# Performance work log

Measured on AMD Instinct MI355X. Metric: run time of the kernel, lower is better.

The kernel has to match this reference:

```python
import jax, jax.numpy as jnp
import numpy as np


def setup_inputs() -> dict:
    key = jax.random.key(0)
    ks = jax.random.split(key, 7)
    OUT, IN, K = 4096, 4096, 2048
    U_STORED, VT_STORED = 512, 1024  # int(0.5*(K//2+1)), int(0.5*(IN//2+1))
    return {
        "x": jax.random.normal(ks[0], (1024, IN), dtype=jnp.float32),
        "U_real": jax.random.normal(ks[1], (OUT, U_STORED), dtype=jnp.float32) * 0.01,
        "U_imag": jax.random.normal(ks[2], (OUT, U_STORED), dtype=jnp.float32) * 0.01,
        "S": jax.random.normal(ks[3], (K,), dtype=jnp.float32) * 0.02,
        "Vt_real": jax.random.normal(ks[4], (K, VT_STORED), dtype=jnp.float32) * 0.01,
        "Vt_imag": jax.random.normal(ks[5], (K, VT_STORED), dtype=jnp.float32) * 0.01,
        "bias": jnp.zeros((OUT,), dtype=jnp.float32),
    }


def _decompress(coeffs_real, coeffs_imag, n):
    # Zero-pad truncated rfft coefficients back to n//2+1, then inverse rfft.
    c = jax.lax.complex(coeffs_real, coeffs_imag)
    num_unique = n // 2 + 1
    pad = num_unique - c.shape[-1]
    if pad > 0:
        c = jnp.pad(c, ((0, 0), (0, pad)))
    elif pad < 0:
        c = c[..., :num_unique]
    return jnp.fft.irfft(c, n=n, axis=-1)


def reference(x, U_real, U_imag, S, Vt_real, Vt_imag, bias):
    k_rank = S.shape[0]
    in_features = x.shape[-1]
    U = _decompress(U_real, U_imag, k_rank)            # (out, k)
    Vh = _decompress(Vt_real, Vt_imag, in_features)    # (k, in)
    W = (U * S[None, :]) @ Vh                          # (out, in) reconstructed weight
    return x @ W.T + bias                              # F.linear(x, W, bias)
```

## Files before the change

kernel.cpp:

```cpp
#include <hip/hip_runtime.h>
#include <math.h>
#include <stdint.h>

#define PI2 6.28318530717958647692f

typedef __bf16 bf16x8 __attribute__((ext_vector_type(8)));
typedef float f32x4 __attribute__((ext_vector_type(4)));

typedef __attribute__((address_space(1))) const void gvoid_t;
typedef __attribute__((address_space(3))) void lvoid_t;

__device__ __forceinline__ void g2l16(const void* g, void* l) {
    __builtin_amdgcn_global_load_lds(
        reinterpret_cast<gvoid_t*>(reinterpret_cast<uintptr_t>(g)),
        reinterpret_cast<lvoid_t*>(reinterpret_cast<uintptr_t>(l)),
        16, 0, 0);
}

__device__ __forceinline__ short f2bf(float f) {
    unsigned u = __float_as_uint(f);
    u += 0x7FFFu + ((u >> 16) & 1u);
    return (short)(u >> 16);
}

__device__ __forceinline__ unsigned pack2bf(float a, float b) {
    return (unsigned)(unsigned short)f2bf(a) |
           ((unsigned)(unsigned short)f2bf(b) << 16);
}

__device__ __forceinline__ float bflo(unsigned v) { return __uint_as_float(v << 16); }
__device__ __forceinline__ float bfhi(unsigned v) { return __uint_as_float(v & 0xFFFF0000u); }

__device__ __forceinline__ int xcd_swizzle(int blk, int G) {
    return (blk & 7) * (G >> 3) + (blk >> 3);
}

__global__ __launch_bounds__(256) void aux_all8(
    const float* __restrict__ x,
    const float* __restrict__ Ur, const float* __restrict__ Ui,
    const float* __restrict__ S,
    const float* __restrict__ Vr, const float* __restrict__ Vi,
    short* __restrict__ xe, short* __restrict__ xo,
    short* __restrict__ B1f, short* __restrict__ VcatT,
    short* __restrict__ B2, short* __restrict__ Ucat)
{
    __shared__ float tlds[64][68];
    const int b   = (int)blockIdx.x;
    const int tid = threadIdx.x;

    if (b < 1024) {
        unsigned i = (b * 256u + tid) * 8u;
        int r = i >> 11, j0 = i & 2047;
        const float* xr = x + (size_t)r * 4096 + j0;
        float4 a0 = ((const float4*)xr)[0], a1 = ((const float4*)xr)[1];
        float4 b0 = ((const float4*)(xr + 2048))[0],
               b1 = ((const float4*)(xr + 2048))[1];
        uint4 oe = {pack2bf(a0.x + b0.x, a0.y + b0.y),
                    pack2bf(a0.z + b0.z, a0.w + b0.w),
                    pack2bf(a1.x + b1.x, a1.y + b1.y),
                    pack2bf(a1.z + b1.z, a1.w + b1.w)};
        *(uint4*)(xe + i) = oe;
        uint4 oo = {pack2bf(a0.x - b0.x, a0.y - b0.y),
                    pack2bf(a0.z - b0.z, a0.w - b0.w),
                    pack2bf(a1.x - b1.x, a1.y - b1.y),
                    pack2bf(a1.z - b1.z, a1.w - b1.w)};
        *(uint4*)(xo + i) = oo;
    } else if (b < 3072) {
        unsigned i = ((b - 1024) * 256u + tid) * 8u;
        int r = i >> 11, j0 = i & 2047;
        const float inv_n = 1.0f / 4096.0f;
        float v[8];
        if (r < 512) {
            if (r == 0) {
                #pragma unroll
                for (int u = 0; u < 8; ++u) v[u] = inv_n;
            } else {
                #pragma unroll
                for (int u = 0; u < 8; ++u) {
                    int t = (r * (j0 + u)) & 2047;
                    v[u] = 2.0f * inv_n * cosf((float)t * (PI2 / 2048.0f));
                }
            }
        } else if (r < 1024) {
            int m = r - 512;
            #pragma unroll
            for (int u = 0; u < 8; ++u) {
                int t = (m * (j0 + u)) & 2047;
                v[u] = -2.0f * inv_n * sinf((float)t * (PI2 / 2048.0f));
            }
        } else if (r < 1536) {
            int c = 2 * (r - 1024) + 1;
            #pragma unroll
            for (int u = 0; u < 8; ++u) {
                int t = (c * (j0 + u)) & 4095;
                v[u] = 2.0f * inv_n * cosf((float)t * (PI2 / 4096.0f));
            }
        } else {
            int m = 2 * (r - 1536) + 1;
            #pragma unroll
            for (int u = 0; u < 8; ++u) {
                int t = (m * (j0 + u)) & 4095;
                v[u] = -2.0f * inv_n * sinf((float)t * (PI2 / 4096.0f));
            }
        }
        uint4 o = {pack2bf(v[0], v[1]), pack2bf(v[2], v[3]),
                   pack2bf(v[4], v[5]), pack2bf(v[6], v[7])};
        *(uint4*)(B1f + i) = o;
    } else if (b < 4096) {
        const int bb  = b - 3072;
        const int m   = bb >> 9;
        const int tt  = bb & 511;
        const int tkk = tt >> 4;
        const int tc  = tt & 15;
        const float* src = (m ? Vi : Vr) + (size_t)(tkk * 64) * 1024 + tc * 64;

        #pragma unroll
        for (int pass = 0; pass < 4; ++pass) {
            int r  = pass * 16 + (tid >> 4);
            int cq = (tid & 15) * 4;
            float4 v = *(const float4*)(src + (size_t)r * 1024 + cq);
            *(float4*)&tlds[r][cq] = v;
        }
        __syncthreads();

        const int cl = tid & 63;
        const int ch = (tid >> 6) * 16;
        const int c  = tc * 64 + cl;
        const int f  = ((c & 1) << 10) + (m << 9) + (c >> 1);
        float vv[16];
        #pragma unroll
        for (int j = 0; j < 16; ++j) vv[j] = tlds[ch + j][cl];
        uint4 o0 = {pack2bf(vv[0],  vv[1]),  pack2bf(vv[2],  vv[3]),
                    pack2bf(vv[4],  vv[5]),  pack2bf(vv[6],  vv[7])};
        uint4 o1 = {pack2bf(vv[8],  vv[9]),  pack2bf(vv[10], vv[11]),
                    pack2bf(vv[12], vv[13]), pack2bf(vv[14], vv[15])};
        uint4* dst = (uint4*)(VcatT + (size_t)f * 2048 + tkk * 64 + ch);
        dst[0] = o0;
        dst[1] = o1;
    } else if (b < 5120) {
        unsigned i = ((b - 4096) * 256u + tid) * 8u;
        int p = i >> 11, k0 = i & 2047;
        float4 s0 = *(const float4*)(S + k0);
        float4 s1 = *(const float4*)(S + k0 + 4);
        float sv[8] = {s0.x, s0.y, s0.z, s0.w, s1.x, s1.y, s1.z, s1.w};
        const float inv_n = 1.0f / 2048.0f;
        float v[8];
        if (p == 0) {
            #pragma unroll
            for (int u = 0; u < 8; ++u) v[u] = inv_n * sv[u];
        } else if (p < 512) {
            #pragma unroll
            for (int u = 0; u < 8; ++u) {
                int t = (p * (k0 + u)) & 2047;
                v[u] = 2.0f * inv_n * cosf((float)t * (PI2 / 2048.0f)) * sv[u];
            }
        } else {
            int q = p - 512;
            #pragma unroll
            for (int u = 0; u < 8; ++u) {
                int t = (q * (k0 + u)) & 2047;
                v[u] = -2.0f * inv_n * sinf((float)t * (PI2 / 2048.0f)) * sv[u];
            }
        }
        uint4 o = {pack2bf(v[0], v[1]), pack2bf(v[2], v[3]),
                   pack2bf(v[4], v[5]), pack2bf(v[6], v[7])};
        *(uint4*)(B2 + i) = o;
    } else {
        unsigned i = ((b - 5120) * 256u + tid) * 8u;
        int o_ = i >> 10, c = i & 1023;
        const float* src = (c < 512) ? (Ur + (size_t)o_ * 512 + c)
                                     : (Ui + (size_t)o_ * 512 + (c - 512));
        float4 a = ((const float4*)src)[0], bq = ((const float4*)src)[1];
        uint4 o = {pack2bf(a.x, a.y), pack2bf(a.z, a.w),
                   pack2bf(bq.x, bq.y), pack2bf(bq.z, bq.w)};
        *(uint4*)(Ucat + i) = o;
    }
}

__device__ __forceinline__ void tile_core(
    const short* __restrict__ A, int lda,
    const short* __restrict__ B, int ldb, int K,
    short* As, short* Bs, int bm, int bn, f32x4 (&acc)[4][4])
{
    const int tid  = threadIdx.x;
    const int wave = tid >> 6;
    const int lane = tid & 63;
    const int wm   = (wave >> 1) << 6;
    const int wn   = (wave & 1) << 6;
    const int l16  = lane & 15;
    const int quad = lane >> 4;
    const int rk   = l16 & 7;

    int aoff[4], boff[4], loff[4];
    #pragma unroll
    for (int p = 0; p < 4; ++p) {
        int L   = p * 256 + wave * 64 + lane;
        int row = L >> 3;
        int swz = (L & 7) ^ (row & 7);
        aoff[p] = (bm + row) * lda + swz * 8;
        boff[p] = (bn + row) * ldb + swz * 8;
        loff[p] = L * 8;
    }

    #pragma unroll
    for (int p = 0; p < 4; ++p) g2l16(A + aoff[p], As + loff[p]);
    #pragma unroll
    for (int p = 0; p < 4; ++p) g2l16(B + boff[p], Bs + loff[p]);
    __syncthreads();

    int cur = 0;
    for (int k0 = 0; k0 < K; k0 += 64) {
        const int nxt = cur ^ 1;
        if (k0 + 64 < K) {
            #pragma unroll
            for (int p = 0; p < 4; ++p)
                g2l16(A + aoff[p] + k0 + 64, As + nxt * 8192 + loff[p]);
            #pragma unroll
            for (int p = 0; p < 4; ++p)
                g2l16(B + boff[p] + k0 + 64, Bs + nxt * 8192 + loff[p]);
        }

        const short* Asc = As + cur * 8192;
        const short* Bsc = Bs + cur * 8192;
        #pragma unroll
        for (int h = 0; h < 2; ++h) {
            const int cs8 = ((((h << 2) | quad) ^ rk) << 3);
            bf16x8 b[4];
            #pragma unroll
            for (int nt = 0; nt < 4; ++nt)
                b[nt] = *(const bf16x8*)(Bsc + (wn + nt * 16 + l16) * 64 + cs8);
            #pragma unroll
            for (int mt = 0; mt < 4; ++mt) {
                bf16x8 a = *(const bf16x8*)(Asc + (wm + mt * 16 + l16) * 64 + cs8);
                #pragma unroll
                for (int nt = 0; nt < 4; ++nt)
                    acc[mt][nt] = __builtin_amdgcn_mfma_f32_16x16x32_bf16(
                        a, b[nt], acc[mt][nt], 0, 0, 0);
            }
        }
        __syncthreads();
        cur = nxt;
    }
}

__device__ __forceinline__ void store_tile_bf16(
    f32x4 (&acc)[4][4], short* __restrict__ C, int ldc, int bm, int bn)
{
    const int tid  = threadIdx.x;
    const int wave = tid >> 6;
    const int lane = tid & 63;
    const int wm   = (wave >> 1) << 6;
    const int wn   = (wave & 1) << 6;
    const int l16  = lane & 15;
    const int quad = lane >> 4;
    #pragma unroll
    for (int nt = 0; nt < 4; ++nt) {
        int col = bn + wn + nt * 16 + l16;
        #pragma unroll
        for (int mt = 0; mt < 4; ++mt) {
            int rowb = bm + wm + mt * 16 + quad * 4;
            #pragma unroll
            for (int r = 0; r < 4; ++r)
                C[(size_t)(rowb + r) * ldc + col] = f2bf(acc[mt][nt][r]);
        }
    }
}

__device__ __forceinline__ void store_frag(
    f32x4 (&acc)[4][4], short* __restrict__ planeTile)
{
    uint4* p = (uint4*)planeTile;
    const int tid = threadIdx.x;
    #pragma unroll
    for (int c = 0; c < 8; ++c) {
        int nt = c >> 1, mt0 = (c & 1) * 2;
        uint4 o = {pack2bf(acc[mt0][nt][0],     acc[mt0][nt][1]),
                   pack2bf(acc[mt0][nt][2],     acc[mt0][nt][3]),
                   pack2bf(acc[mt0 + 1][nt][0], acc[mt0 + 1][nt][1]),
                   pack2bf(acc[mt0 + 1][nt][2], acc[mt0 + 1][nt][3])};
        p[c * 256 + tid] = o;
    }
}

template <bool OUT_F32>
__device__ __forceinline__ void reduce_unit(
    const short* __restrict__ P, size_t planeU4, int SK,
    int tile, int c, int tilesX, void* __restrict__ Out, int ldc,
    const float* __restrict__ bias)
{
    const int bm = (tile / tilesX) << 7;
    const int bn = (tile % tilesX) << 7;
    const int tid  = threadIdx.x;
    const int wave = tid >> 6;
    const int lane = tid & 63;
    const int wm   = (wave >> 1) << 6;
    const int wn   = (wave & 1) << 6;
    const int l16  = lane & 15;
    const int quad = lane >> 4;
    const int nt   = c >> 1, mt0 = (c & 1) * 2;

    const uint4* P4 = (const uint4*)P;
    const size_t base = (size_t)tile * 2048 + (size_t)c * 256 + tid;
    float f[8] = {0, 0, 0, 0, 0, 0, 0, 0};
    for (int z = 0; z < SK; ++z) {
        uint4 v = P4[(size_t)z * planeU4 + base];
        f[0] += bflo(v.x); f[1] += bfhi(v.x);
        f[2] += bflo(v.y); f[3] += bfhi(v.y);
        f[4] += bflo(v.z); f[5] += bfhi(v.z);
        f[6] += bflo(v.w); f[7] += bfhi(v.w);
    }
    const int col = bn + wn + nt * 16 + l16;
    float bv = 0.f;
    if (OUT_F32) bv = bias[col];
    #pragma unroll
    for (int j = 0; j < 8; ++j) {
        int mt  = mt0 + (j >> 2);
        int row = bm + wm + mt * 16 + quad * 4 + (j & 3);
        if (OUT_F32)
            ((float*)Out)[(size_t)row * ldc + col] = f[j] + bv;
        else
            ((short*)Out)[(size_t)row * ldc + col] = f2bf(f[j]);
    }
}

__global__ __launch_bounds__(256, 2) void gemm_s1w2(
    const short* __restrict__ xe, const short* __restrict__ xo,
    const short* __restrict__ B1f,
    const short* __restrict__ B2, const short* __restrict__ VcatT,
    short* __restrict__ P, short* __restrict__ PW)
{
    __shared__ __align__(16) short As[2 * 128 * 64];
    __shared__ __align__(16) short Bs[2 * 128 * 64];

    f32x4 acc[4][4];
    #pragma unroll
    for (int i = 0; i < 4; ++i)
        #pragma unroll
        for (int j = 0; j < 4; ++j)
            acc[i][j] = (f32x4){0.f, 0.f, 0.f, 0.f};

    const int raw = (int)blockIdx.x;
    if (raw < 512) {
        const int u    = xcd_swizzle(raw, 512);
        const int z    = u >> 7;
        const int tile = u & 127;
        const int tx   = tile & 15, ty = tile >> 4;
        const bool odd = (tx & 8) != 0;
        const short* A = (odd ? xo : xe) + (size_t)z * 512;
        const short* B = B1f + (odd ? (size_t)1024 * 2048 : 0) + (size_t)z * 512;
        const int bm   = ty << 7;
        const int bn   = (tx & 7) << 7;

        tile_core(A, 2048, B, 2048, 512, As, Bs, bm, bn, acc);
        store_frag(acc, P + (size_t)z * 2097152 + (size_t)tile * 16384);
    } else {
        const int u    = xcd_swizzle(raw - 512, 512);
        const int z    = u >> 7;
        const int tile = u & 127;
        const int bm   = (tile >> 4) << 7;
        const int bn   = (tile & 15) << 7;

        tile_core(B2 + (size_t)z * 512, 2048, VcatT + (size_t)z * 512, 2048,
                  512, As, Bs, bm, bn, acc);
        store_frag(acc, PW + (size_t)z * 2097152 + (size_t)tile * 16384);
    }
}

__global__ __launch_bounds__(256) void reduce_s1w2(
    const short* __restrict__ P, const short* __restrict__ PW,
    short* __restrict__ Xp, short* __restrict__ W2)
{
    const int b   = (int)blockIdx.x;
    const int sub = b & 1023;
    if (b < 1024)
        reduce_unit<false>(P,  (size_t)2097152 >> 3, 4, sub >> 3, sub & 7,
                           16, Xp, 2048, nullptr);
    else
        reduce_unit<false>(PW, (size_t)2097152 >> 3, 4, sub >> 3, sub & 7,
                           16, W2, 2048, nullptr);
}

__global__ __launch_bounds__(256, 2) void gemm_sk_frag(
    const short* __restrict__ A, int lda,
    const short* __restrict__ B, int ldb,
    short* __restrict__ P, size_t planeShorts, int Kpart,
    int tileShift, int tilesXShift)
{
    __shared__ __align__(16) short As[2 * 128 * 64];
    __shared__ __align__(16) short Bs[2 * 128 * 64];

    f32x4 acc[4][4];
    #pragma unroll
    for (int i = 0; i < 4; ++i)
        #pragma unroll
        for (int j = 0; j < 4; ++j)
            acc[i][j] = (f32x4){0.f, 0.f, 0.f, 0.f};

    const int u    = xcd_swizzle((int)blockIdx.x, (int)gridDim.x);
    const int z    = u >> tileShift;
    const int tile = u & ((1 << tileShift) - 1);
    const int bm   = (tile >> tilesXShift) << 7;
    const int bn   = (tile & ((1 << tilesXShift) - 1)) << 7;

    tile_core(A + (size_t)z * Kpart, lda, B + (size_t)z * Kpart, ldb, Kpart,
              As, Bs, bm, bn, acc);
    store_frag(acc, P + (size_t)z * planeShorts + (size_t)tile * 16384);
}

template <bool OUT_F32>
__global__ __launch_bounds__(256) void reduce_frag(
    const short* __restrict__ P, size_t planeShorts, int SK,
    int tilesX, void* __restrict__ Out, int ldc,
    const float* __restrict__ bias)
{
    reduce_unit<OUT_F32>(P, planeShorts >> 3, SK,
                         (int)(blockIdx.x >> 3), (int)(blockIdx.x & 7),
                         tilesX, Out, ldc, bias);
}

template <bool OUT_F32>
__global__ __launch_bounds__(256, 2) void gemm_direct(
    const short* __restrict__ A, int lda,
    const short* __restrict__ B, int ldb,
    void* __restrict__ Cv, int ldc,
    const float* __restrict__ bias, int K)
{
    __shared__ __align__(16) short As[2 * 128 * 64];
    __shared__ __align__(16) short Bs[2 * 128 * 64];

    f32x4 acc[4][4];
    #pragma unroll
    for (int i = 0; i < 4; ++i)
        #pragma unroll
        for (int j = 0; j < 4; ++j)
            acc[i][j] = (f32x4){0.f, 0.f, 0.f, 0.f};

    const int bm = blockIdx.y << 7;
    const int bn = blockIdx.x << 7;
    tile_core(A, lda, B, ldb, K, As, Bs, bm, bn, acc);

    const int tid  = threadIdx.x;
    const int wave = tid >> 6;
    const int lane = tid & 63;
    const int wm   = (wave >> 1) << 6;
    const int wn   = (wave & 1) << 6;
    const int l16  = lane & 15;
    const int quad = lane >> 4;

    if (OUT_F32) {
        float* C = (float*)Cv;
        #pragma unroll
        for (int nt = 0; nt < 4; ++nt) {
            int col = bn + wn + nt * 16 + l16;
            float bv = bias ? bias[col] : 0.f;
            #pragma unroll
            for (int mt = 0; mt < 4; ++mt) {
                int rowb = bm + wm + mt * 16 + quad * 4;
                #pragma unroll
                for (int r = 0; r < 4; ++r)
                    C[(size_t)(rowb + r) * ldc + col] = acc[mt][nt][r] + bv;
            }
        }
    } else {
        store_tile_bf16(acc, (short*)Cv, ldc, bm, bn);
    }
}

__global__ __launch_bounds__(256, 2) void gemm_s1f_dir(
    const short* __restrict__ xe, const short* __restrict__ xo,
    const short* __restrict__ B1f, short* __restrict__ Xp)
{
    __shared__ __align__(16) short As[2 * 128 * 64];
    __shared__ __align__(16) short Bs[2 * 128 * 64];

    f32x4 acc[4][4];
    #pragma unroll
    for (int i = 0; i < 4; ++i)
        #pragma unroll
        for (int j = 0; j < 4; ++j)
            acc[i][j] = (f32x4){0.f, 0.f, 0.f, 0.f};

    const int u    = (int)blockIdx.x;
    const int tx   = u & 15, ty = u >> 4;
    const bool odd = (tx & 8) != 0;
    const short* A = odd ? xo : xe;
    const short* B = B1f + (odd ? (size_t)1024 * 2048 : 0);
    const int bm   = ty << 7;
    const int bn   = (tx & 7) << 7;

    tile_core(A, 2048, B, 2048, 2048, As, Bs, bm, bn, acc);
    store_tile_bf16(acc, Xp, 2048, bm, bn + (odd ? 1024 : 0));
}

extern "C" void kernel_launch(void* const* d_in, const int* in_sizes, int n_in,
                              void* d_out, int out_size, void* d_ws, size_t ws_size,
                              hipStream_t stream) {
    const float* x    = (const float*)d_in[0];
    const float* Ur   = (const float*)d_in[1];
    const float* Ui   = (const float*)d_in[2];
    const float* S    = (const float*)d_in[3];
    const float* Vr   = (const float*)d_in[4];
    const float* Vi   = (const float*)d_in[5];
    const float* bias = (const float*)d_in[6];
    float* out = (float*)d_out;

    short* ws    = (short*)d_ws;
    short* xe    = ws;
    short* xo    = xe    + (size_t)1024 * 2048;
    short* B1f   = xo    + (size_t)1024 * 2048;
    short* VcatT = B1f   + (size_t)2048 * 2048;
    short* B2    = VcatT + (size_t)2048 * 2048;
    short* Ucat  = B2    + (size_t)1024 * 2048;
    short* Xp    = Ucat  + (size_t)4096 * 1024;
    short* W2    = Xp    + (size_t)1024 * 2048;
    short* Gm    = W2    + (size_t)1024 * 2048;
    short* Pp    = Gm    + (size_t)1024 * 1024;
    short* PW    = Pp    + (size_t)8388608;

    const size_t need = (size_t)((char*)(PW + (size_t)8388608) - (char*)d_ws);

    aux_all8<<<dim3(7168), 256, 0, stream>>>(
        x, Ur, Ui, S, Vr, Vi, xe, xo, B1f, VcatT, B2, Ucat);

    if (ws_size >= need) {
        gemm_s1w2<<<dim3(1024), 256, 0, stream>>>(
            xe, xo, B1f, B2, VcatT, Pp, PW);
        reduce_s1w2<<<dim3(2048), 256, 0, stream>>>(Pp, PW, Xp, W2);

        gemm_sk_frag<<<dim3(512), 256, 0, stream>>>(
            Xp, 2048, W2, 2048, Pp, (size_t)1048576, 256, 6, 3);
        reduce_frag<false><<<dim3(512), 256, 0, stream>>>(
            Pp, (size_t)1048576, 8, 8, Gm, 1024, nullptr);

        gemm_sk_frag<<<dim3(512), 256, 0, stream>>>(
            Gm, 1024, Ucat, 1024, Pp, (size_t)4194304, 512, 8, 5);
        reduce_frag<true><<<dim3(2048), 256, 0, stream>>>(
            Pp, (size_t)4194304, 2, 32, out, 4096, bias);
    } else {
        gemm_s1f_dir<<<dim3(128), 256, 0, stream>>>(xe, xo, B1f, Xp);
        gemm_direct<false><<<dim3(16, 8), 256, 0, stream>>>(
            B2, 2048, VcatT, 2048, W2, 2048, nullptr, 2048);
        gemm_direct<false><<<dim3(8, 8), 256, 0, stream>>>(
            Xp, 2048, W2, 2048, Gm, 1024, nullptr, 2048);
        gemm_direct<true><<<dim3(32, 8), 256, 0, stream>>>(
            Gm, 1024, Ucat, 1024, out, 4096, bias, 1024);
    }
}
```

Before: 169.7 us.

## Apply even/odd FFT split to U-side DFT, halving W2 GEMM reduction depth

Folds S into the Vt transpose and splits it into even and odd sums and differences (VSe/VSo), so the B2 DFT basis becomes half-size even/odd-frequency blocks. The W2 GEMM now contracts over 1024 instead of 2048, with each row block choosing VSe or VSo. Ucat columns are reordered to match by splitting the even and odd interleaved entries, and the aux grid shrinks. This halves the FLOPs and traffic of the W2 stage, at the cost of strided float2 gathers in the Ucat build and extra work in the transpose blocks.

```diff
diff --git a/kernel.cpp b/kernel.cpp
--- a/kernel.cpp
+++ b/kernel.cpp
@@ -41,10 +41,12 @@
     const float* __restrict__ S,
     const float* __restrict__ Vr, const float* __restrict__ Vi,
     short* __restrict__ xe, short* __restrict__ xo,
-    short* __restrict__ B1f, short* __restrict__ VcatT,
+    short* __restrict__ B1f, short* __restrict__ VSe, short* __restrict__ VSo,
     short* __restrict__ B2, short* __restrict__ Ucat)
 {
-    __shared__ float tlds[64][68];
+    __shared__ float tlds0[64][68];
+    __shared__ float tlds1[64][68];
+    __shared__ float s_lo[64], s_hi[64];
     const int b   = (int)blockIdx.x;
     const int tid = threadIdx.x;
 
@@ -106,20 +108,25 @@
         uint4 o = {pack2bf(v[0], v[1]), pack2bf(v[2], v[3]),
                    pack2bf(v[4], v[5]), pack2bf(v[6], v[7])};
         *(uint4*)(B1f + i) = o;
-    } else if (b < 4096) {
+    } else if (b < 3584) {
         const int bb  = b - 3072;
-        const int m   = bb >> 9;
-        const int tt  = bb & 511;
+        const int m   = bb >> 8;
+        const int tt  = bb & 255;
         const int tkk = tt >> 4;
         const int tc  = tt & 15;
-        const float* src = (m ? Vi : Vr) + (size_t)(tkk * 64) * 1024 + tc * 64;
+        const float* srcA = (m ? Vi : Vr) + (size_t)(tkk * 64) * 1024 + tc * 64;
+        const float* srcB = srcA + (size_t)1024 * 1024;
 
         #pragma unroll
         for (int pass = 0; pass < 4; ++pass) {
             int r  = pass * 16 + (tid >> 4);
             int cq = (tid & 15) * 4;
-            float4 v = *(const float4*)(src + (size_t)r * 1024 + cq);
-            *(float4*)&tlds[r][cq] = v;
+            *(float4*)&tlds0[r][cq] = *(const float4*)(srcA + (size_t)r * 1024 + cq);
+            *(float4*)&tlds1[r][cq] = *(const float4*)(srcB + (size_t)r * 1024 + cq);
+        }
+        if (tid < 64) {
+            s_lo[tid] = S[tkk * 64 + tid];
+            s_hi[tid] = S[tkk * 64 + tid + 1024];
         }
         __syncthreads();
 
@@ -127,52 +134,80 @@
         const int ch = (tid >> 6) * 16;
         const int c  = tc * 64 + cl;
         const int f  = ((c & 1) << 10) + (m << 9) + (c >> 1);
-        float vv[16];
-        #pragma unroll
-        for (int j = 0; j < 16; ++j) vv[j] = tlds[ch + j][cl];
-        uint4 o0 = {pack2bf(vv[0],  vv[1]),  pack2bf(vv[2],  vv[3]),
-                    pack2bf(vv[4],  vv[5]),  pack2bf(vv[6],  vv[7])};
-        uint4 o1 = {pack2bf(vv[8],  vv[9]),  pack2bf(vv[10], vv[11]),
-                    pack2bf(vv[12], vv[13]), pack2bf(vv[14], vv[15])};
-        uint4* dst = (uint4*)(VcatT + (size_t)f * 2048 + tkk * 64 + ch);
-        dst[0] = o0;
-        dst[1] = o1;
-    } else if (b < 5120) {
-        unsigned i = ((b - 4096) * 256u + tid) * 8u;
-        int p = i >> 11, k0 = i & 2047;
-        float4 s0 = *(const float4*)(S + k0);
-        float4 s1 = *(const float4*)(S + k0 + 4);
-        float sv[8] = {s0.x, s0.y, s0.z, s0.w, s1.x, s1.y, s1.z, s1.w};
+        float ve[16], vo[16];
+        #pragma unroll
+        for (int j = 0; j < 16; ++j) {
+            float a  = tlds0[ch + j][cl] * s_lo[ch + j];
+            float bb2 = tlds1[ch + j][cl] * s_hi[ch + j];
+            ve[j] = a + bb2;
+            vo[j] = a - bb2;
+        }
+        uint4* de = (uint4*)(VSe + (size_t)f * 1024 + tkk * 64 + ch);
+        de[0] = (uint4){pack2bf(ve[0],  ve[1]),  pack2bf(ve[2],  ve[3]),
+                        pack2bf(ve[4],  ve[5]),  pack2bf(ve[6],  ve[7])};
+        de[1] = (uint4){pack2bf(ve[8],  ve[9]),  pack2bf(ve[10], ve[11]),
+                        pack2bf(ve[12], ve[13]), pack2bf(ve[14], ve[15])};
+        uint4* dox = (uint4*)(VSo + (size_t)f * 1024 + tkk * 64 + ch);
+        dox[0] = (uint4){pack2bf(vo[0],  vo[1]),  pack2bf(vo[2],  vo[3]),
+                         pack2bf(vo[4],  vo[5]),  pack2bf(vo[6],  vo[7])};
+        dox[1] = (uint4){pack2bf(vo[8],  vo[9]),  pack2bf(vo[10], vo[11]),
+                         pack2bf(vo[12], vo[13]), pack2bf(vo[14], vo[15])};
+    } else if (b < 4096) {
+        unsigned i = ((b - 3584) * 256u + tid) * 8u;
+        int p = i >> 10, k0 = i & 1023;
+        int grp = p >> 8, pp = p & 255;
         const float inv_n = 1.0f / 2048.0f;
         float v[8];
-        if (p == 0) {
-            #pragma unroll
-            for (int u = 0; u < 8; ++u) v[u] = inv_n * sv[u];
-        } else if (p < 512) {
+        if (grp == 0) {
+            if (p == 0) {
+                #pragma unroll
+                for (int u = 0; u < 8; ++u) v[u] = inv_n;
+            } else {
+                #pragma unroll
+                for (int u = 0; u < 8; ++u) {
+                    int t = (pp * (k0 + u)) & 1023;
+                    v[u] = 2.0f * inv_n * cosf((float)t * (PI2 / 1024.0f));
+                }
+            }
+        } else if (grp == 1) {
             #pragma unroll
             for (int u = 0; u < 8; ++u) {
-                int t = (p * (k0 + u)) & 2047;
-                v[u] = 2.0f * inv_n * cosf((float)t * (PI2 / 2048.0f)) * sv[u];
-            }
-        } else {
-            int q = p - 512;
+                int t = (pp * (k0 + u)) & 1023;
+                v[u] = -2.0f * inv_n * sinf((float)t * (PI2 / 1024.0f));
+            }
+        } else if (grp == 2) {
+            int q = 2 * pp + 1;
             #pragma unroll
             for (int u = 0; u < 8; ++u) {
                 int t = (q * (k0 + u)) & 2047;
-                v[u] = -2.0f * inv_n * sinf((float)t * (PI2 / 2048.0f)) * sv[u];
+                v[u] = 2.0f * inv_n * cosf((float)t * (PI2 / 2048.0f));
+            }
+        } else {
+            int q = 2 * pp + 1;
+            #pragma unroll
+            for (int u = 0; u < 8; ++u) {
+                int t = (q * (k0 + u)) & 2047;
+                v[u] = -2.0f * inv_n * sinf((float)t * (PI2 / 2048.0f));
             }
         }
         uint4 o = {pack2bf(v[0], v[1]), pack2bf(v[2], v[3]),
                    pack2bf(v[4], v[5]), pack2bf(v[6], v[7])};
         *(uint4*)(B2 + i) = o;
     } else {
-        unsigned i = ((b - 5120) * 256u + tid) * 8u;
+        unsigned i = ((b - 4096) * 256u + tid) * 8u;
         int o_ = i >> 10, c = i & 1023;
-        const float* src = (c < 512) ? (Ur + (size_t)o_ * 512 + c)
-                                     : (Ui + (size_t)o_ * 512 + (c - 512));
-        float4 a = ((const float4*)src)[0], bq = ((const float4*)src)[1];
-        uint4 o = {pack2bf(a.x, a.y), pack2bf(a.z, a.w),
-                   pack2bf(bq.x, bq.y), pack2bf(bq.z, bq.w)};
+        int grp = c >> 8, cc = c & 255;
+        int par = grp >> 1;
+        const float2* s2 = (const float2*)(((grp & 1) ? Ui : Ur)
+                                           + (size_t)o_ * 512 + 2 * cc);
+        float v[8];
+        #pragma unroll
+        for (int j = 0; j < 8; ++j) {
+            float2 q = s2[j];
+            v[j] = par ? q.y : q.x;
+        }
+        uint4 o = {pack2bf(v[0], v[1]), pack2bf(v[2], v[3]),
+                   pack2bf(v[4], v[5]), pack2bf(v[6], v[7])};
         *(uint4*)(Ucat + i) = o;
     }
 }
@@ -326,7 +361,8 @@
 __global__ __launch_bounds__(256, 2) void gemm_s1w2(
     const short* __restrict__ xe, const short* __restrict__ xo,
     const short* __restrict__ B1f,
-    const short* __restrict__ B2, const short* __restrict__ VcatT,
+    const short* __restrict__ B2,
+    const short* __restrict__ VSe, const short* __restrict__ VSo,
     short* __restrict__ P, short* __restrict__ PW)
 {
     __shared__ __align__(16) short As[2 * 128 * 64];
@@ -359,9 +395,10 @@
         const int tile = u & 127;
         const int bm   = (tile >> 4) << 7;
         const int bn   = (tile & 15) << 7;
-
-        tile_core(B2 + (size_t)z * 512, 2048, VcatT + (size_t)z * 512, 2048,
-                  512, As, Bs, bm, bn, acc);
+        const short* Bv = (bm < 512) ? VSe : VSo;
+
+        tile_core(B2 + (size_t)z * 256, 1024, Bv + (size_t)z * 256, 1024,
+                  256, As, Bs, bm, bn, acc);
         store_frag(acc, PW + (size_t)z * 2097152 + (size_t)tile * 16384);
     }
 }
@@ -508,9 +545,10 @@
     short* xe    = ws;
     short* xo    = xe    + (size_t)1024 * 2048;
     short* B1f   = xo    + (size_t)1024 * 2048;
-    short* VcatT = B1f   + (size_t)2048 * 2048;
-    short* B2    = VcatT + (size_t)2048 * 2048;
-    short* Ucat  = B2    + (size_t)1024 * 2048;
+    short* VSe   = B1f   + (size_t)2048 * 2048;
+    short* VSo   = VSe   + (size_t)2048 * 1024;
+    short* B2    = VSo   + (size_t)2048 * 1024;
+    short* Ucat  = B2    + (size_t)1024 * 1024;
     short* Xp    = Ucat  + (size_t)4096 * 1024;
     short* W2    = Xp    + (size_t)1024 * 2048;
     short* Gm    = W2    + (size_t)1024 * 2048;
@@ -519,12 +557,12 @@
 
     const size_t need = (size_t)((char*)(PW + (size_t)8388608) - (char*)d_ws);
 
-    aux_all8<<<dim3(7168), 256, 0, stream>>>(
-        x, Ur, Ui, S, Vr, Vi, xe, xo, B1f, VcatT, B2, Ucat);
+    aux_all8<<<dim3(6144), 256, 0, stream>>>(
+        x, Ur, Ui, S, Vr, Vi, xe, xo, B1f, VSe, VSo, B2, Ucat);
 
     if (ws_size >= need) {
         gemm_s1w2<<<dim3(1024), 256, 0, stream>>>(
-            xe, xo, B1f, B2, VcatT, Pp, PW);
+            xe, xo, B1f, B2, VSe, VSo, Pp, PW);
         reduce_s1w2<<<dim3(2048), 256, 0, stream>>>(Pp, PW, Xp, W2);
 
         gemm_sk_frag<<<dim3(512), 256, 0, stream>>>(
@@ -538,8 +576,11 @@
             Pp, (size_t)4194304, 2, 32, out, 4096, bias);
     } else {
         gemm_s1f_dir<<<dim3(128), 256, 0, stream>>>(xe, xo, B1f, Xp);
-        gemm_direct<false><<<dim3(16, 8), 256, 0, stream>>>(
-            B2, 2048, VcatT, 2048, W2, 2048, nullptr, 2048);
+        gemm_direct<false><<<dim3(16, 4), 256, 0, stream>>>(
+            B2, 1024, VSe, 1024, W2, 2048, nullptr, 1024);
+        gemm_direct<false><<<dim3(16, 4), 256, 0, stream>>>(
+            B2 + (size_t)512 * 1024, 1024, VSo, 1024,
+            W2 + (size_t)512 * 2048, 2048, nullptr, 1024);
         gemm_direct<false><<<dim3(8, 8), 256, 0, stream>>>(
             Xp, 2048, W2, 2048, Gm, 1024, nullptr, 2048);
         gemm_direct<true><<<dim3(32, 8), 256, 0, stream>>>(
```

New measurement: 165.7 us. 1.02x faster.
